# Performance work log

Measured on AMD Instinct MI355X. Metric: run time of the kernel, lower is better.

The kernel has to match this reference:

```python
import jax, jax.numpy as jnp
import numpy as np

FS = 3          # filter_size
B, C, H, W = 16, 256, 96, 96
BN_EPS = 1e-5


def setup_inputs() -> dict:
    key = jax.random.key(0)
    ks = jax.random.split(key, 6)
    s = 0.05
    return {
        "x": jax.random.normal(ks[0], (B, C, H, W), jnp.float32),
        "convoluted": jax.random.normal(ks[1], (B, C, H, W), jnp.float32),
        # filter_gen_conv: 1x1 Conv2d(C -> C)
        "w_gen": jax.random.normal(ks[2], (C, C, 1, 1), jnp.float32) * s,
        "b_gen": jax.random.normal(ks[3], (C,), jnp.float32) * s,
        # c1: 3x3 Conv2d(C -> C) + BatchNorm2d(C) + ReLU
        "w_c1": jax.random.normal(ks[4], (C, C, 3, 3), jnp.float32) * s,
        "b_c1": jax.random.normal(ks[5], (C,), jnp.float32) * s,
        "gamma": jnp.ones((C,), jnp.float32),
        "beta": jnp.zeros((C,), jnp.float32),
    }


def reference(x, convoluted, w_gen, b_gen, w_c1, b_c1, gamma, beta):
    b, c, h, w = x.shape
    # adaptive_avg_pool2d(x, FS): H,W divisible by FS -> uniform bins
    pooled = x.reshape(b, c, FS, h // FS, FS, w // FS).mean(axis=(3, 5))  # [b,c,FS,FS]
    # 1x1 conv generating per-sample per-channel filters
    gen = jnp.einsum('bcij,oc->boij', pooled, w_gen[:, :, 0, 0]) + b_gen[None, :, None, None]

    # c1: conv3x3 (pad 1) + BatchNorm (training-mode batch stats) + ReLU
    y = jax.lax.conv_general_dilated(
        convoluted, w_c1, window_strides=(1, 1), padding=((1, 1), (1, 1)),
        dimension_numbers=('NCHW', 'OIHW', 'NCHW')) + b_c1[None, :, None, None]
    mu = y.mean(axis=(0, 2, 3), keepdims=True)
    var = y.var(axis=(0, 2, 3), keepdims=True)
    y = (y - mu) * jax.lax.rsqrt(var + BN_EPS)
    y = jax.nn.relu(y * gamma[None, :, None, None] + beta[None, :, None, None])

    # dynamic per-sample depthwise conv: groups = b*c, symmetric pad (FS odd)
    y = y.reshape(1, b * c, h, w)
    filt = gen.reshape(b * c, 1, FS, FS)
    pad = (FS - 1) // 2
    out = jax.lax.conv_general_dilated(
        y, filt, window_strides=(1, 1), padding=((pad, pad), (pad, pad)),
        feature_group_count=b * c, dimension_numbers=('NCHW', 'OIHW', 'NCHW'))
    return out.reshape(b, c, h, w)
```

## Files before the change

### kernel.cpp

```cpp
#include <hip/hip_runtime.h>

typedef __bf16 bf16x8 __attribute__((ext_vector_type(8)));
typedef float f32x4 __attribute__((ext_vector_type(4)));

static __device__ __forceinline__ ushort f2b(float f) {
    uint32_t x = __float_as_uint(f);
    x += 0x7fffu + ((x >> 16) & 1u);
    return (ushort)(x >> 16);
}
static __device__ __forceinline__ float b2f(ushort u) {
    return __uint_as_float(((uint32_t)u) << 16);
}

typedef const __attribute__((address_space(1))) uint32_t gu32;
typedef __attribute__((address_space(3))) uint32_t lu32;
static __device__ __forceinline__ void gl_lds16(const void* g, void* l) {
    __builtin_amdgcn_global_load_lds((gu32*)g, (lu32*)l, 16, 0, 0);
}

__global__ __launch_bounds__(256) void pool_k(const float* __restrict__ x,
                                              float* __restrict__ pooled) {
    const int bc  = blockIdx.x;
    const int tid = threadIdx.x;
    const int lane = tid & 63, wv = tid >> 6;
    const float4* p4 = (const float4*)(x + (size_t)bc * 9216);
    __shared__ float red[4][9];
#pragma unroll
    for (int bi = 0; bi < 3; ++bi) {
#pragma unroll
        for (int bj = 0; bj < 3; ++bj) {
            int row = bi * 32 + (tid >> 3);
            int c4  = bj * 8 + (tid & 7);
            float4 f = p4[row * 24 + c4];
            float s = f.x + f.y + f.z + f.w;
#pragma unroll
            for (int off = 32; off; off >>= 1) s += __shfl_down(s, off);
            if (lane == 0) red[wv][bi * 3 + bj] = s;
        }
    }
    __syncthreads();
    if (tid < 9) {
        float s = red[0][tid] + red[1][tid] + red[2][tid] + red[3][tid];
        pooled[(size_t)bc * 9 + tid] = s * (1.0f / 1024.0f);
    }
}

__global__ __launch_bounds__(256) void gen_k(const float* __restrict__ pooled,
                                             const float* __restrict__ wgen,
                                             const float* __restrict__ bgen,
                                             float* __restrict__ gen) {
    __shared__ float pl[256];
    const int b = blockIdx.x / 9, ij = blockIdx.x % 9;
    const int o = threadIdx.x;
    pl[o] = pooled[((size_t)b * 256 + o) * 9 + ij];
    __syncthreads();
    float a = bgen[o];
    const float4* wg4 = (const float4*)(wgen + (size_t)o * 256);
    const float4* pl4 = (const float4*)pl;
#pragma unroll 4
    for (int q = 0; q < 64; ++q) {
        float4 w = wg4[q], p = pl4[q];
        a += w.x * p.x + w.y * p.y + w.z * p.z + w.w * p.w;
    }
    gen[((size_t)b * 256 + o) * 9 + ij] = a;
}

__global__ __launch_bounds__(256) void wtr_k(const float* __restrict__ wc1,
                                             ushort* __restrict__ wtr) {
    int g = blockIdx.x * 256 + threadIdx.x;
    int step = g >> 10;
    int row  = (g >> 2) & 255;
    int c8   = g & 3;
    int ch = step / 9, tap = step - ch * 9;
    int cb = ch * 32 + c8 * 8;
    ushort tmp[8];
#pragma unroll
    for (int j = 0; j < 8; ++j)
        tmp[j] = f2b(wc1[(size_t)row * 2304 + (size_t)(cb + j) * 9 + tap]);
    *(uint4*)(wtr + (size_t)g * 8) = *(const uint4*)tmp;
}

__global__ __launch_bounds__(512) void xt_k(const float* __restrict__ xin,
                                            ushort* __restrict__ xt,
                                            ushort* __restrict__ zeros) {
    __shared__ ushort T[96][258];
    const int bh = blockIdx.x;
    const int b = bh / 96, h = bh % 96;
    const int tid = threadIdx.x;
    const float* src = xin + (size_t)b * 2359296 + (size_t)h * 96;
#pragma unroll
    for (int it = 0; it < 12; ++it) {
        int id = tid + it * 512;
        int c = id / 24, q = id - c * 24;
        float4 v = *(const float4*)(src + (size_t)c * 9216 + q * 4);
        int px = q * 4;
        T[px + 0][c] = f2b(v.x); T[px + 1][c] = f2b(v.y);
        T[px + 2][c] = f2b(v.z); T[px + 3][c] = f2b(v.w);
    }
    __syncthreads();
    ushort* dst = xt + (size_t)bh * 24576;
#pragma unroll
    for (int it = 0; it < 12; ++it) {
        int id = tid + it * 512;
        int px = id >> 6, cq = id & 63;
        ushort4 u;
        u.x = T[px][cq * 4 + 0]; u.y = T[px][cq * 4 + 1];
        u.z = T[px][cq * 4 + 2]; u.w = T[px][cq * 4 + 3];
        *(ushort4*)(dst + px * 256 + cq * 4) = u;
    }
    if (bh == 0) {
        uint4 zz; zz.x = zz.y = zz.z = zz.w = 0u;
        *(uint4*)(zeros + (size_t)tid * 8) = zz;
    }
}

__global__ __launch_bounds__(256, 2) void conv_k(const ushort* __restrict__ xt,
                                                 const ushort* __restrict__ wtr,
                                                 const float* __restrict__ bc1,
                                                 const ushort* __restrict__ zeros,
                                                 ushort* __restrict__ yb,
                                                 float* __restrict__ part) {
    __shared__ ushort Bl[2][9408];

    const int blk0 = blockIdx.x;
    const int blk = (blk0 & 7) * 192 + (blk0 >> 3);
    const int b = blk / 96, h = blk % 96;
    const int tid = threadIdx.x;
    const int lane = tid & 63, wv = tid >> 6;
    const int lo = lane & 15, hi = lane >> 4;

#pragma unroll
    for (int z0 = 0; z0 < 2; ++z0) {
        int z = tid + z0 * 256;
        if (z < 384) {
            int bsel = z >= 192, rem = z - bsel * 192;
            int row = rem >> 6, pxp = ((rem >> 5) & 1) ? 97 : 0, c = rem & 31;
            Bl[bsel][(row * 98 + pxp) * 32 + c] = 0;
        }
    }

    const int laneoff = (lane >> 2) * 256 + (lane & 3) * 8;

    auto stage = [&](int chunk, int buf) {
#pragma unroll
        for (int j = 0; j < 5; ++j) {
            const int s = wv + j * 4;
            if (s < 18) {
                const int row = s / 6, pseg = s - (s / 6) * 6;
                const int r = h + row - 1;
                const ushort* base = ((unsigned)r < 96u)
                    ? (xt + ((size_t)(b * 96 + r) * 96 + pseg * 16) * 256
                          + chunk * 32)
                    : zeros;
                gl_lds16(base + laneoff,
                         &Bl[buf][(row * 98 + 1 + pseg * 16) * 32]);
            }
        }
    };

    const uint4* Abase = (const uint4*)wtr + ((wv * 64 + lo) * 4 + hi);

    f32x4 acc[4][6] = {};
    uint4 abuf[3][4];

    stage(0, 0);
#pragma unroll
    for (int mi = 0; mi < 4; ++mi) abuf[0][mi] = Abase[mi * 64];
#pragma unroll
    for (int mi = 0; mi < 4; ++mi) abuf[1][mi] = (Abase + 1024)[mi * 64];
    __syncthreads();

    for (int k = 0; k < 4; ++k) {
#pragma unroll
        for (int t = 0; t < 18; ++t) {
            if (t == 0) stage(2 * k + 1, 1);
            else if (t == 9 && k < 3) stage(2 * k + 2, 0);
            if (t < 16 || k < 3) {
                const uint4* Ap = Abase + (size_t)(k * 18 + t + 2) * 1024;
#pragma unroll
                for (int mi = 0; mi < 4; ++mi)
                    abuf[(t + 2) % 3][mi] = Ap[mi * 64];
            }
            const int tap = (t < 9) ? t : t - 9;
            const int dy = tap / 3, dx = tap % 3;
            const ushort* Bp = &Bl[t >= 9][(dy * 98 + lo + dx) * 32 + hi * 8];
            bf16x8 bfr[6];
#pragma unroll
            for (int ni = 0; ni < 6; ++ni)
                bfr[ni] = *(const bf16x8*)(Bp + ni * 512);
#pragma unroll
            for (int mi = 0; mi < 4; ++mi) {
                const bf16x8 af = *(const bf16x8*)&abuf[t % 3][mi];
#pragma unroll
                for (int ni = 0; ni < 6; ++ni)
                    acc[mi][ni] = __builtin_amdgcn_mfma_f32_16x16x32_bf16(
                        af, bfr[ni], acc[mi][ni], 0, 0, 0);
            }
            if (t == 8) __syncthreads();
            else if (t == 17 && k < 3) __syncthreads();
        }
    }

    const size_t ybase = (size_t)blk * 24576;
#pragma unroll
    for (int mi = 0; mi < 4; ++mi) {
        float s[4], s2[4];
#pragma unroll
        for (int rr = 0; rr < 4; ++rr) {
            const int o = wv * 64 + mi * 16 + hi * 4 + rr;
            const float bias = bc1[o];
            float sv = 0.f, sv2 = 0.f;
#pragma unroll
            for (int ni = 0; ni < 6; ++ni) {
                const int px = ni * 16 + lo;
                float v = acc[mi][ni][rr] + bias;
                yb[ybase + o * 96 + px] = f2b(v);
                sv += v; sv2 += v * v;
            }
            s[rr] = sv; s2[rr] = sv2;
        }
#pragma unroll
        for (int off = 1; off < 16; off <<= 1) {
#pragma unroll
            for (int rr = 0; rr < 4; ++rr) {
                s[rr]  += __shfl_xor(s[rr], off);
                s2[rr] += __shfl_xor(s2[rr], off);
            }
        }
        if (lo == 0) {
#pragma unroll
            for (int rr = 0; rr < 4; ++rr) {
                const int o = wv * 64 + mi * 16 + hi * 4 + rr;
                part[(size_t)o * 1536 + blk]          = s[rr];
                part[393216 + (size_t)o * 1536 + blk] = s2[rr];
            }
        }
    }
}

__global__ __launch_bounds__(256) void bnred_k(const float* __restrict__ part,
                                               const float* __restrict__ gamma,
                                               const float* __restrict__ beta,
                                               float* __restrict__ bnp) {
    const int o = blockIdx.x, t = threadIdx.x;
    const float* p0 = part + (size_t)o * 1536;
    const float* p1 = p0 + 393216;
    float s = 0.f, s2 = 0.f;
#pragma unroll
    for (int k = 0; k < 6; ++k) { s += p0[t + k * 256]; s2 += p1[t + k * 256]; }
    const int lane = t & 63, wv = t >> 6;
#pragma unroll
    for (int off = 32; off; off >>= 1) {
        s  += __shfl_down(s, off);
        s2 += __shfl_down(s2, off);
    }
    __shared__ float r1[4], r2[4];
    if (lane == 0) { r1[wv] = s; r2[wv] = s2; }
    __syncthreads();
    if (t == 0) {
        float S  = r1[0] + r1[1] + r1[2] + r1[3];
        float S2 = r2[0] + r2[1] + r2[2] + r2[3];
        const float invN = 1.0f / 147456.0f;
        float mu  = S * invN;
        float var = S2 * invN - mu * mu;
        float sc  = gamma[o] * rsqrtf(var + 1e-5f);
        bnp[o]       = sc;
        bnp[256 + o] = beta[o] - mu * sc;
    }
}

__global__ __launch_bounds__(256) void dw_k(const ushort* __restrict__ yb,
                                            const float* __restrict__ gen,
                                            const float* __restrict__ bnp,
                                            float* __restrict__ out) {
    __shared__ float pl[9216];
    const int bc = blockIdx.x, tid = threadIdx.x;
    const int b = bc >> 8, c = bc & 255;
    const float sc = bnp[c], sh = bnp[256 + c];
    const ushort4* yb4 = (const ushort4*)yb;
    const size_t pbase = (size_t)b * 589824 + c * 24;
#pragma unroll
    for (int it = 0; it < 9; ++it) {
        int e4 = tid + it * 256;
        int row = e4 / 24, px4 = e4 - row * 24;
        ushort4 u = yb4[pbase + (size_t)row * 6144 + px4];
        float4 f;
        f.x = fmaxf(b2f(u.x) * sc + sh, 0.f);
        f.y = fmaxf(b2f(u.y) * sc + sh, 0.f);
        f.z = fmaxf(b2f(u.z) * sc + sh, 0.f);
        f.w = fmaxf(b2f(u.w) * sc + sh, 0.f);
        *(float4*)&pl[e4 * 4] = f;
    }
    float g[9];
    const float* gp = gen + (size_t)bc * 9;
#pragma unroll
    for (int k = 0; k < 9; ++k) g[k] = gp[k];
    __syncthreads();
    float* op = out + (size_t)bc * 9216;
#pragma unroll
    for (int it = 0; it < 36; ++it) {
        int i = tid + it * 256;
        int row = i / 96, col = i - row * 96;
        float a = 0.f;
#pragma unroll
        for (int dy = 0; dy < 3; ++dy) {
            int rr = row + dy - 1;
            if (rr < 0 || rr >= 96) continue;
#pragma unroll
            for (int dxq = 0; dxq < 3; ++dxq) {
                int cc = col + dxq - 1;
                if (cc < 0 || cc >= 96) continue;
                a += pl[rr * 96 + cc] * g[dy * 3 + dxq];
            }
        }
        op[i] = a;
    }
}

extern "C" void kernel_launch(void* const* d_in, const int* in_sizes, int n_in,
                              void* d_out, int out_size, void* d_ws, size_t ws_size,
                              hipStream_t stream) {
    const float* x       = (const float*)d_in[0];
    const float* conv_in = (const float*)d_in[1];
    const float* w_gen   = (const float*)d_in[2];
    const float* b_gen   = (const float*)d_in[3];
    const float* w_c1    = (const float*)d_in[4];
    const float* b_c1    = (const float*)d_in[5];
    const float* gamma   = (const float*)d_in[6];
    const float* beta    = (const float*)d_in[7];
    float* out = (float*)d_out;

    char* ws = (char*)d_ws;
    float*  pooled = (float*)(ws + 0);
    float*  gen    = (float*)(ws + 147456);
    ushort* wtr    = (ushort*)(ws + 294912);
    float*  part   = (float*)(ws + 1474560);
    float*  bnp    = (float*)(ws + 4620288);
    ushort* zeros  = (ushort*)(ws + 4622336);
    ushort* yb     = (ushort*)(ws + 4630528);
    ushort* xt     = (ushort*)d_out;

    pool_k <<<4096, 256, 0, stream>>>(x, pooled);
    gen_k  <<<144,  256, 0, stream>>>(pooled, w_gen, b_gen, gen);
    wtr_k  <<<288,  256, 0, stream>>>(w_c1, wtr);
    xt_k   <<<1536, 512, 0, stream>>>(conv_in, xt, zeros);
    conv_k <<<1536, 256, 0, stream>>>(xt, wtr, b_c1, zeros, yb, part);
    bnred_k<<<256,  256, 0, stream>>>(part, gamma, beta, bnp);
    dw_k   <<<4096, 256, 0, stream>>>(yb, gen, bnp, out);
}
```

Before: 340.0 us.

## Split conv blocks over output-channel halves; vectorize depthwise conv with padded LDS

The 3x3 conv kernel now launches twice as many blocks. Each block computes half of the output channels for one image row, which halves the accumulator and A-fragment registers and raises the launch-bounds occupancy hint from 2 to 3. In exchange, the input row tile is staged into LDS twice, once per channel half, which adds redundant global-to-LDS traffic. Separately, the depthwise kernel now stores a zero-padded LDS tile and computes four outputs per thread with float4 reads and stores, removing per-pixel bounds checks and scalar stores.

```diff
diff --git a/kernel.cpp b/kernel.cpp
--- a/kernel.cpp
+++ b/kernel.cpp
@@ -114,7 +114,7 @@
     }
 }
 
-__global__ __launch_bounds__(256, 2) void conv_k(const ushort* __restrict__ xt,
+__global__ __launch_bounds__(256, 3) void conv_k(const ushort* __restrict__ xt,
                                                  const ushort* __restrict__ wtr,
                                                  const float* __restrict__ bc1,
                                                  const ushort* __restrict__ zeros,
@@ -123,8 +123,9 @@
     __shared__ ushort Bl[2][9408];
 
     const int blk0 = blockIdx.x;
-    const int blk = (blk0 & 7) * 192 + (blk0 >> 3);
-    const int b = blk / 96, h = blk % 96;
+    const int blk = (blk0 & 7) * 384 + (blk0 >> 3);
+    const int ohalf = blk & 1, rowblk = blk >> 1;
+    const int b = rowblk / 96, h = rowblk % 96;
     const int tid = threadIdx.x;
     const int lane = tid & 63, wv = tid >> 6;
     const int lo = lane & 15, hi = lane >> 4;
@@ -158,16 +159,17 @@
         }
     };
 
-    const uint4* Abase = (const uint4*)wtr + ((wv * 64 + lo) * 4 + hi);
-
-    f32x4 acc[4][6] = {};
-    uint4 abuf[3][4];
+    const uint4* Abase =
+        (const uint4*)wtr + ((ohalf * 128 + wv * 32 + lo) * 4 + hi);
+
+    f32x4 acc[2][6] = {};
+    uint4 abuf[3][2];
 
     stage(0, 0);
 #pragma unroll
-    for (int mi = 0; mi < 4; ++mi) abuf[0][mi] = Abase[mi * 64];
-#pragma unroll
-    for (int mi = 0; mi < 4; ++mi) abuf[1][mi] = (Abase + 1024)[mi * 64];
+    for (int mi = 0; mi < 2; ++mi) abuf[0][mi] = Abase[mi * 64];
+#pragma unroll
+    for (int mi = 0; mi < 2; ++mi) abuf[1][mi] = (Abase + 1024)[mi * 64];
     __syncthreads();
 
     for (int k = 0; k < 4; ++k) {
@@ -178,7 +180,7 @@
             if (t < 16 || k < 3) {
                 const uint4* Ap = Abase + (size_t)(k * 18 + t + 2) * 1024;
 #pragma unroll
-                for (int mi = 0; mi < 4; ++mi)
+                for (int mi = 0; mi < 2; ++mi)
                     abuf[(t + 2) % 3][mi] = Ap[mi * 64];
             }
             const int tap = (t < 9) ? t : t - 9;
@@ -189,7 +191,7 @@
             for (int ni = 0; ni < 6; ++ni)
                 bfr[ni] = *(const bf16x8*)(Bp + ni * 512);
 #pragma unroll
-            for (int mi = 0; mi < 4; ++mi) {
+            for (int mi = 0; mi < 2; ++mi) {
                 const bf16x8 af = *(const bf16x8*)&abuf[t % 3][mi];
 #pragma unroll
                 for (int ni = 0; ni < 6; ++ni)
@@ -201,13 +203,13 @@
         }
     }
 
-    const size_t ybase = (size_t)blk * 24576;
-#pragma unroll
-    for (int mi = 0; mi < 4; ++mi) {
+    const size_t ybase = (size_t)rowblk * 24576;
+#pragma unroll
+    for (int mi = 0; mi < 2; ++mi) {
         float s[4], s2[4];
 #pragma unroll
         for (int rr = 0; rr < 4; ++rr) {
-            const int o = wv * 64 + mi * 16 + hi * 4 + rr;
+            const int o = ohalf * 128 + wv * 32 + mi * 16 + hi * 4 + rr;
             const float bias = bc1[o];
             float sv = 0.f, sv2 = 0.f;
 #pragma unroll
@@ -230,9 +232,9 @@
         if (lo == 0) {
 #pragma unroll
             for (int rr = 0; rr < 4; ++rr) {
-                const int o = wv * 64 + mi * 16 + hi * 4 + rr;
-                part[(size_t)o * 1536 + blk]          = s[rr];
-                part[393216 + (size_t)o * 1536 + blk] = s2[rr];
+                const int o = ohalf * 128 + wv * 32 + mi * 16 + hi * 4 + rr;
+                part[(size_t)o * 1536 + rowblk]          = s[rr];
+                part[393216 + (size_t)o * 1536 + rowblk] = s2[rr];
             }
         }
     }
@@ -273,47 +275,63 @@
                                             const float* __restrict__ gen,
                                             const float* __restrict__ bnp,
                                             float* __restrict__ out) {
-    __shared__ float pl[9216];
+    __shared__ float pl[98][104];
     const int bc = blockIdx.x, tid = threadIdx.x;
     const int b = bc >> 8, c = bc & 255;
     const float sc = bnp[c], sh = bnp[256 + c];
+
+#pragma unroll
+    for (int z0 = 0; z0 < 4; ++z0) {
+        int z = tid + z0 * 256;
+        if (z < 104) pl[0][z] = 0.f;
+        else if (z < 208) pl[97][z - 104] = 0.f;
+        else if (z < 976) {
+            int w = z - 208;
+            int r = (w >> 3) + 1, j = w & 7;
+            pl[r][(j < 4) ? j : 96 + j] = 0.f;
+        }
+    }
+
     const ushort4* yb4 = (const ushort4*)yb;
     const size_t pbase = (size_t)b * 589824 + c * 24;
 #pragma unroll
     for (int it = 0; it < 9; ++it) {
         int e4 = tid + it * 256;
-        int row = e4 / 24, px4 = e4 - row * 24;
-        ushort4 u = yb4[pbase + (size_t)row * 6144 + px4];
+        int row = e4 / 24, q = e4 - row * 24;
+        ushort4 u = yb4[pbase + (size_t)row * 6144 + q];
         float4 f;
         f.x = fmaxf(b2f(u.x) * sc + sh, 0.f);
         f.y = fmaxf(b2f(u.y) * sc + sh, 0.f);
         f.z = fmaxf(b2f(u.z) * sc + sh, 0.f);
         f.w = fmaxf(b2f(u.w) * sc + sh, 0.f);
-        *(float4*)&pl[e4 * 4] = f;
+        *(float4*)&pl[row + 1][q * 4 + 4] = f;
     }
     float g[9];
     const float* gp = gen + (size_t)bc * 9;
 #pragma unroll
     for (int k = 0; k < 9; ++k) g[k] = gp[k];
     __syncthreads();
-    float* op = out + (size_t)bc * 9216;
-#pragma unroll
-    for (int it = 0; it < 36; ++it) {
-        int i = tid + it * 256;
-        int row = i / 96, col = i - row * 96;
-        float a = 0.f;
+
+    float4* op4 = (float4*)(out + (size_t)bc * 9216);
+#pragma unroll
+    for (int it = 0; it < 9; ++it) {
+        int e4 = tid + it * 256;
+        int row = e4 / 24, q = e4 - row * 24;
+        float4 o4 = {0.f, 0.f, 0.f, 0.f};
 #pragma unroll
         for (int dy = 0; dy < 3; ++dy) {
-            int rr = row + dy - 1;
-            if (rr < 0 || rr >= 96) continue;
-#pragma unroll
-            for (int dxq = 0; dxq < 3; ++dxq) {
-                int cc = col + dxq - 1;
-                if (cc < 0 || cc >= 96) continue;
-                a += pl[rr * 96 + cc] * g[dy * 3 + dxq];
-            }
-        }
-        op[i] = a;
+            const float4* pr = (const float4*)&pl[row + dy][0];
+            float4 x0 = pr[q];
+            float4 x1 = pr[q + 1];
+            float4 x2 = pr[q + 2];
+            const float w0 = g[dy * 3 + 0], w1 = g[dy * 3 + 1],
+                        w2 = g[dy * 3 + 2];
+            o4.x += w0 * x0.w + w1 * x1.x + w2 * x1.y;
+            o4.y += w0 * x1.x + w1 * x1.y + w2 * x1.z;
+            o4.z += w0 * x1.y + w1 * x1.z + w2 * x1.w;
+            o4.w += w0 * x1.z + w1 * x1.w + w2 * x2.x;
+        }
+        op4[e4] = o4;
     }
 }
 
@@ -344,7 +362,7 @@
     gen_k  <<<144,  256, 0, stream>>>(pooled, w_gen, b_gen, gen);
     wtr_k  <<<288,  256, 0, stream>>>(w_c1, wtr);
     xt_k   <<<1536, 512, 0, stream>>>(conv_in, xt, zeros);
-    conv_k <<<1536, 256, 0, stream>>>(xt, wtr, b_c1, zeros, yb, part);
+    conv_k <<<3072, 256, 0, stream>>>(xt, wtr, b_c1, zeros, yb, part);
     bnred_k<<<256,  256, 0, stream>>>(part, gamma, beta, bnp);
     dw_k   <<<4096, 256, 0, stream>>>(yb, gen, bnp, out);
 }
```

New measurement: 315.3 us. 1.08x faster.
